# Optimization experiments

Hardware: AMD Instinct MI355X
Metric: run time of the kernel (lower is better)

## Reference

```python
import jax, jax.numpy as jnp
import numpy as np

B = 131072
SEQ = 64
HID = 20
LSTM_W_BITS = 8
LSTM_A_BITS = 6
LIN_W_BITS = 8
LIN_A_BITS = 6
IO_BITS = 8


def _ste(x, q):
    # straight-through estimator: forward value q, gradient of identity
    return x + jax.lax.stop_gradient(q - x)


def fq_signed_dyn(x, bits):
    # symmetric per-tensor fake quant, dynamic max-abs scale
    qmax = 2.0 ** (bits - 1) - 1.0
    s = jnp.maximum(jnp.max(jnp.abs(x)), 1e-8) / qmax
    q = jnp.clip(jnp.round(x / s), -qmax, qmax) * s
    return _ste(x, q)


def fq_unsigned_dyn(x, bits):
    # unsigned per-tensor fake quant (for post-ReLU activations)
    qmax = 2.0 ** bits - 1.0
    s = jnp.maximum(jnp.max(x), 1e-8) / qmax
    q = jnp.clip(jnp.round(x / s), 0.0, qmax) * s
    return _ste(x, q)


def fq_sigmoid(x, bits):
    # quantized sigmoid: output in [0,1], fixed scale 1/(2^b-1)
    qmax = 2.0 ** bits - 1.0
    y = jax.nn.sigmoid(x)
    return _ste(y, jnp.round(y * qmax) / qmax)


def fq_tanh(x, bits):
    # quantized tanh: output in [-1,1], fixed scale 1/(2^(b-1)-1)
    qmax = 2.0 ** (bits - 1) - 1.0
    y = jnp.tanh(x)
    return _ste(y, jnp.round(y * qmax) / qmax)


def setup_inputs() -> dict:
    key = jax.random.key(0)
    ks = jax.random.split(key, 10)

    def u(k, shape, fan_in):
        lim = 1.0 / np.sqrt(fan_in)
        return jax.random.uniform(k, shape, jnp.float32, -lim, lim)

    x = jax.random.normal(ks[0], (B, SEQ), jnp.float32)
    w_ih = u(ks[1], (4 * HID, 1), HID)      # LSTM input weights (input_size=1)
    w_hh = u(ks[2], (4 * HID, HID), HID)    # LSTM recurrent weights
    b = u(ks[3], (4 * HID,), HID)           # combined bias (bias_quant=None)
    W1 = u(ks[4], (64, HID), HID)
    b1 = u(ks[5], (64,), HID)
    W2 = u(ks[6], (32, 64), 64)
    b2 = u(ks[7], (32,), 64)
    W3 = u(ks[8], (4, 32), 32)
    b3 = u(ks[9], (4,), 32)
    return dict(x=x, w_ih=w_ih, w_hh=w_hh, b=b, W1=W1, b1=b1, W2=W2, b2=b2, W3=W3, b3=b3)


def reference(x, w_ih, w_hh, b, W1, b1, W2, b2, W3, b3):
    # io_quant (Int8ActPerTensorFloat) on LSTM input
    xq = fq_signed_dyn(x, IO_BITS)
    w_ih_q = fq_signed_dyn(w_ih, LSTM_W_BITS)
    w_hh_q = fq_signed_dyn(w_hh, LSTM_W_BITS)

    xs = xq.reshape(B, SEQ, 1).transpose(1, 0, 2)  # (SEQ, B, 1)

    def step(carry, x_t):
        h, c = carry
        gates = x_t @ w_ih_q.T + h @ w_hh_q.T + b   # (B, 4*HID)
        gates = fq_signed_dyn(gates, LSTM_A_BITS)   # gate_acc quant
        i_g, f_g, g_g, o_g = jnp.split(gates, 4, axis=-1)
        i = fq_sigmoid(i_g, LSTM_A_BITS)
        f = fq_sigmoid(f_g, LSTM_A_BITS)
        g = fq_tanh(g_g, LSTM_A_BITS)
        o = fq_sigmoid(o_g, LSTM_A_BITS)
        c_new = fq_signed_dyn(f * c + i * g, LSTM_A_BITS)  # cell_state quant
        h_new = o * fq_tanh(c_new, LSTM_A_BITS)
        return (h_new, c_new), None

    h0 = jnp.zeros((B, HID), jnp.float32)
    (h_last, _), _ = jax.lax.scan(step, (h0, h0), xs)

    # quantized MLP head: QuantReLU -> QuantLinear x3 -> ReLU
    out = fq_unsigned_dyn(jax.nn.relu(h_last), LIN_A_BITS)
    out = out @ fq_signed_dyn(W1, LIN_W_BITS).T + b1
    out = fq_unsigned_dyn(jax.nn.relu(out), LIN_A_BITS)
    out = out @ fq_signed_dyn(W2, LIN_W_BITS).T + b2
    out = fq_unsigned_dyn(jax.nn.relu(out), LIN_A_BITS)
    out = out @ fq_signed_dyn(W3, LIN_W_BITS).T + b3
    return jax.nn.relu(out)
```

## Files before the change

### kernel.cpp

```cpp
#include <hip/hip_runtime.h>
#include <math.h>


#define NBLK  256
#define NTHR  512
#define SEQL  64
#define HIDN  20
#define G4    80

typedef float f2 __attribute__((ext_vector_type(2)));
typedef unsigned long long u64;

__device__ __forceinline__ float tanh_xla(float x){
  const float kClamp = 7.90531110763549805f;
  float xc = fminf(fmaxf(x, -kClamp), kClamp);
  float x2 = xc*xc;
  float p = fmaf(x2, -2.76076847742355e-16f, 2.00018790482477e-13f);
  p = fmaf(x2, p, -8.60467152213735e-11f);
  p = fmaf(x2, p,  5.12229709037114e-08f);
  p = fmaf(x2, p,  1.48572235717979e-05f);
  p = fmaf(x2, p,  6.37261928875436e-04f);
  p = fmaf(x2, p,  4.89352455891786e-03f);
  p = p * xc;
  float q = fmaf(x2, 1.19825839466702e-06f, 1.18534705686654e-04f);
  q = fmaf(x2, q, 2.26843463243900e-03f);
  q = fmaf(x2, q, 4.89352518554385e-03f);
  float y = p / q;
  return (fabsf(x) < 4e-4f) ? x : y;
}

__device__ __forceinline__ float qround(float x, float s, float inv_s, float tol){
  float n = rintf(__fmul_rn(x, inv_s));
  float e = fmaf(-n, s, x);
  if (__builtin_expect(fabsf(fabsf(e) - 0.5f*s) <= tol*s, 0))
    n = rintf(x / s);
  return n;
}

__device__ __forceinline__ float phase_max(float lmax, int phase,
                                           u64* slots, int blk, int tid,
                                           volatile u64* s_red64,
                                           volatile u64* s_bc64)
{
  #pragma unroll
  for (int off=32; off; off>>=1) lmax = fmaxf(lmax, __shfl_xor(lmax, off, 64));
  const int wid = tid>>6, lane = tid&63;
  const unsigned int tag = (unsigned int)(phase+1);
  const u64 tw = ((u64)tag)<<32;
  if (lane==0) s_red64[wid] = tw | (u64)__float_as_uint(lmax);
  if (wid==0) {
    u64 pv = 0;
    if (lane<8) { do { pv = s_red64[lane]; } while ((unsigned int)(pv>>32)!=tag); }
    float bm = (lane<8) ? __uint_as_float((unsigned int)pv) : 0.f;
    bm = fmaxf(bm, __shfl_xor(bm,4,64));
    bm = fmaxf(bm, __shfl_xor(bm,2,64));
    bm = fmaxf(bm, __shfl_xor(bm,1,64));
    u64* sp = slots + (size_t)(phase&1)*NBLK;
    if (lane==0)
      __hip_atomic_store(sp+blk, tw | (u64)__float_as_uint(bm),
                         __ATOMIC_RELAXED, __HIP_MEMORY_SCOPE_AGENT);
    u64 v0,v1,v2,v3;
    for (;;) {
      v0 = __hip_atomic_load(sp+lane,     __ATOMIC_RELAXED, __HIP_MEMORY_SCOPE_AGENT);
      v1 = __hip_atomic_load(sp+lane+64,  __ATOMIC_RELAXED, __HIP_MEMORY_SCOPE_AGENT);
      v2 = __hip_atomic_load(sp+lane+128, __ATOMIC_RELAXED, __HIP_MEMORY_SCOPE_AGENT);
      v3 = __hip_atomic_load(sp+lane+192, __ATOMIC_RELAXED, __HIP_MEMORY_SCOPE_AGENT);
      bool ok = ((unsigned int)(v0>>32)==tag) && ((unsigned int)(v1>>32)==tag) &&
                ((unsigned int)(v2>>32)==tag) && ((unsigned int)(v3>>32)==tag);
      if (__all(ok)) break;
      __builtin_amdgcn_s_sleep(1);
    }
    unsigned int m0 = (unsigned int)v0, m1 = (unsigned int)v1;
    unsigned int m2 = (unsigned int)v2, m3 = (unsigned int)v3;
    unsigned int m = m0>m1?m0:m1; if (m2>m) m=m2; if (m3>m) m=m3;
    #pragma unroll
    for (int off=32; off; off>>=1) {
      unsigned int o = (unsigned int)__shfl_xor((int)m, off, 64);
      if (o>m) m=o;
    }
    if (lane==0) *s_bc64 = tw | (u64)m;
  }
  u64 bv;
  do { bv = *s_bc64; } while ((unsigned int)(bv>>32)!=tag);
  return __uint_as_float((unsigned int)bv);
}

__global__ void kinit(float* __restrict__ ws) {
  int i = threadIdx.x;
  for (; i < 1152; i += 256) ws[i] = 0.0f;
}

__global__ void kmaxabs_x(const float4* __restrict__ x4, int n4, int* __restrict__ xmax_bits) {
  float m = 0.f;
  int stride = gridDim.x*blockDim.x;
  for (int i = blockIdx.x*blockDim.x + threadIdx.x; i < n4; i += stride) {
    float4 v = x4[i];
    m = fmaxf(fmaxf(fabsf(v.x),fabsf(v.y)), fmaxf(fmaxf(fabsf(v.z),fabsf(v.w)), m));
  }
  #pragma unroll
  for (int off=32; off; off>>=1) m = fmaxf(m, __shfl_xor(m, off, 64));
  __shared__ float red[4];
  int wid = threadIdx.x>>6, lane = threadIdx.x&63;
  if (lane==0) red[wid]=m;
  __syncthreads();
  if (threadIdx.x==0) {
    float bm = fmaxf(fmaxf(red[0],red[1]), fmaxf(red[2],red[3]));
    atomicMax(xmax_bits, __float_as_int(bm));
  }
}

__global__ void kscales(const float* __restrict__ wih, const float* __restrict__ whh,
                        const float* __restrict__ W1, const float* __restrict__ W2,
                        const float* __restrict__ W3, float* __restrict__ ws)
{
  int wid = threadIdx.x>>6, lane = threadIdx.x&63;
  const float* p; int n;
  if      (wid==0){p=wih;n=80;}   else if (wid==1){p=whh;n=1600;}
  else if (wid==2){p=W1;n=1280;}  else if (wid==3){p=W2;n=2048;}
  else            {p=W3;n=128;}
  float m=0.f;
  for (int i=lane;i<n;i+=64) m=fmaxf(m,fabsf(p[i]));
  #pragma unroll
  for (int off=32; off; off>>=1) m=fmaxf(m,__shfl_xor(m,off,64));
  if (lane==0) ws[9+wid]=fmaxf(m,1e-8f)/127.0f;
  if (threadIdx.x==0) {
    float xm = __int_as_float(((const int*)ws)[0]);
    ws[8]=fmaxf(xm,1e-8f)/127.0f;
  }
}

__global__ void __launch_bounds__(NTHR, 2)
kmain(const float* __restrict__ x, const float* __restrict__ w_ih,
      const float* __restrict__ w_hh, const float* __restrict__ bias,
      const float* __restrict__ W1, const float* __restrict__ b1,
      const float* __restrict__ W2, const float* __restrict__ b2,
      const float* __restrict__ W3, const float* __restrict__ b3,
      float* __restrict__ out, float* __restrict__ ws)
{
  __shared__ float s_whh[HIDN*G4];
  __shared__ float s_wih[G4];
  __shared__ float s_b[G4];
  __shared__ float s_W1[HIDN*64];
  __shared__ float s_b1v[64];
  __shared__ float s_W2[64*32];
  __shared__ float s_b2v[32];
  __shared__ float s_W3[32*4];
  __shared__ float s_b3v[4];
  __shared__ float s_lutsig[63];
  __shared__ float s_luttg[63];
  __shared__ float s_luttc[63];
  __shared__ u64 s_red64[8];
  __shared__ u64 s_bc64;

  const int tid = threadIdx.x;
  const int blk = blockIdx.x;
  u64* slots = (u64*)(ws + 64);

  const float sx   = ws[8];
  const float swih = ws[9];
  const float swhh = ws[10];
  const float sw1  = ws[11];
  const float sw2  = ws[12];
  const float sw3  = ws[13];

  for (int i = tid; i < G4; i += NTHR) {
    s_wih[i] = fminf(fmaxf(rintf(w_ih[i]/swih), -127.f), 127.f)*swih;
    s_b[i]   = bias[i];
  }
  for (int i = tid; i < HIDN*G4; i += NTHR) {
    int j = i/HIDN, k = i - j*HIDN;
    s_whh[k*G4+j] = fminf(fmaxf(rintf(w_hh[i]/swhh), -127.f), 127.f)*swhh;
  }
  for (int i = tid; i < 64*HIDN; i += NTHR) {
    int j = i/HIDN, k = i - j*HIDN;
    s_W1[k*64+j] = fminf(fmaxf(rintf(W1[i]/sw1), -127.f), 127.f)*sw1;
  }
  for (int i = tid; i < 32*64; i += NTHR) {
    int j = i>>6, k = i&63;
    s_W2[k*32+j] = fminf(fmaxf(rintf(W2[i]/sw2), -127.f), 127.f)*sw2;
  }
  for (int i = tid; i < 4*32; i += NTHR) {
    int j = i>>5, k = i&31;
    s_W3[k*4+j] = fminf(fmaxf(rintf(W3[i]/sw3), -127.f), 127.f)*sw3;
  }
  if (tid < 64) s_b1v[tid] = b1[tid];
  if (tid < 32) s_b2v[tid] = b2[tid];
  if (tid < 4)  s_b3v[tid] = b3[tid];
  __syncthreads();

  const long bI = (long)blk*NTHR + tid;
  const float* xrow = x + bI*SEQL;
  const float inv_sx = __builtin_amdgcn_rcpf(sx);

  float h[HIDN], c[HIDN];
  #pragma unroll
  for (int k=0;k<HIDN;++k){ h[k]=0.f; c[k]=0.f; }

  float4 x4v;
  #pragma unroll 1
  for (int t=0; t<SEQL; ++t) {
    if ((t&3)==0) x4v = *(const float4*)(xrow + t);
    float xv = (t&3)==1 ? x4v.y : ((t&3)==2 ? x4v.z : ((t&3)==3 ? x4v.w : x4v.x));
    float xq = __fmul_rn(fminf(fmaxf(qround(xv, sx, inv_sx, 1e-4f), -127.f), 127.f), sx);

    f2 hw2[40];
    #pragma unroll
    for (int j=0;j<40;++j) { hw2[j].x = 0.f; hw2[j].y = 0.f; }
    #pragma unroll
    for (int k=0;k<HIDN;++k) {
      float hk = h[k];
      f2 hk2; hk2.x = hk; hk2.y = hk;
      const float4* w4 = (const float4*)&s_whh[k*G4];
      #pragma unroll
      for (int j4=0;j4<20;++j4) {
        float4 w = w4[j4];
        f2 wlo; wlo.x = w.x; wlo.y = w.y;
        f2 whi; whi.x = w.z; whi.y = w.w;
        hw2[2*j4]   = __builtin_elementwise_fma(hk2, wlo, hw2[2*j4]);
        hw2[2*j4+1] = __builtin_elementwise_fma(hk2, whi, hw2[2*j4+1]);
      }
    }
    float* hw = (float*)hw2;
    float lm = 0.f;
    #pragma unroll
    for (int j4=0;j4<20;++j4) {
      float4 wi = *(const float4*)&s_wih[j4*4];
      float4 bb = *(const float4*)&s_b[j4*4];
      float g0 = __fadd_rn(__fadd_rn(__fmul_rn(xq, wi.x), hw[j4*4  ]), bb.x);
      float g1 = __fadd_rn(__fadd_rn(__fmul_rn(xq, wi.y), hw[j4*4+1]), bb.y);
      float g2 = __fadd_rn(__fadd_rn(__fmul_rn(xq, wi.z), hw[j4*4+2]), bb.z);
      float g3 = __fadd_rn(__fadd_rn(__fmul_rn(xq, wi.w), hw[j4*4+3]), bb.w);
      hw[j4*4  ]=g0; hw[j4*4+1]=g1; hw[j4*4+2]=g2; hw[j4*4+3]=g3;
      lm = fmaxf(lm, fmaxf(fmaxf(fabsf(g0),fabsf(g1)), fmaxf(fabsf(g2),fabsf(g3))));
    }
    float gm = phase_max(lm, 2*t, slots, blk, tid, s_red64, &s_bc64);
    float s1 = fmaxf(gm, 1e-8f)/31.0f;
    float inv1 = __builtin_amdgcn_rcpf(s1);

    if (tid < 63) {
      float q  = __fmul_rn((float)(tid-31), s1);
      float ti = tanh_xla(0.5f*q);
      int ni = (int)rintf(fmaf(0.5f, ti, 0.5f)*63.0f);
      ni = min(max(ni,0),63);
      s_lutsig[tid] = (float)ni/63.0f;
    } else if (tid >= 64 && tid < 127) {
      int n = tid - 64 - 31;
      float q  = __fmul_rn((float)n, s1);
      float tg = tanh_xla(q);
      int ng = (int)rintf(tg*31.0f);
      ng = min(max(ng,-31),31);
      s_luttg[tid-64] = (float)ng/31.0f;
    }
    __syncthreads();

    float og[HIDN];
    float lm2 = 0.f;
    #pragma unroll
    for (int k=0;k<HIDN;++k) {
      int ii = min(max((int)qround(hw[k   ], s1, inv1, 2e-5f),-31),31)+31;
      int fi = min(max((int)qround(hw[20+k], s1, inv1, 2e-5f),-31),31)+31;
      int gi = min(max((int)qround(hw[40+k], s1, inv1, 2e-5f),-31),31)+31;
      int oi = min(max((int)qround(hw[60+k], s1, inv1, 2e-5f),-31),31)+31;
      float iv = s_lutsig[ii];
      float fv = s_lutsig[fi];
      float gv = s_luttg[gi];
      og[k]    = s_lutsig[oi];
      float pc = __fadd_rn(__fmul_rn(fv, c[k]), __fmul_rn(iv, gv));
      c[k] = pc;
      lm2 = fmaxf(lm2, fabsf(pc));
    }
    float gm2 = phase_max(lm2, 2*t+1, slots, blk, tid, s_red64, &s_bc64);
    float s2 = fmaxf(gm2, 1e-8f)/31.0f;
    float inv2 = __builtin_amdgcn_rcpf(s2);
    if (tid < 63) {
      float q  = __fmul_rn((float)(tid-31), s2);
      float tc = tanh_xla(q);
      int nc = (int)rintf(tc*31.0f);
      nc = min(max(nc,-31),31);
      s_luttc[tid] = (float)nc/31.0f;
    }
    __syncthreads();
    #pragma unroll
    for (int k=0;k<HIDN;++k) {
      int m = min(max((int)qround(c[k], s2, inv2, 2e-5f),-31),31);
      float cn = __fmul_rn((float)m, s2);
      c[k] = cn;
      h[k] = __fmul_rn(og[k], s_luttc[m+31]);
    }
  }

  float lm3 = 0.f;
  float a0[HIDN];
  #pragma unroll
  for (int k=0;k<HIDN;++k){ float r = fmaxf(h[k],0.f); a0[k]=r; lm3=fmaxf(lm3,r); }
  float gm3 = phase_max(lm3, 128, slots, blk, tid, s_red64, &s_bc64);
  float s3 = fmaxf(gm3,1e-8f)/63.0f;
  float inv3 = __builtin_amdgcn_rcpf(s3);
  #pragma unroll
  for (int k=0;k<HIDN;++k)
    a0[k] = __fmul_rn(fminf(fmaxf(qround(a0[k], s3, inv3, 4e-5f),0.f),63.f), s3);

  float o1[64];
  #pragma unroll
  for (int j=0;j<64;++j) o1[j] = 0.f;
  #pragma unroll
  for (int k=0;k<HIDN;++k) {
    float ak = a0[k];
    #pragma unroll
    for (int j=0;j<64;j+=4) {
      float4 w = *(const float4*)&s_W1[k*64+j];
      o1[j]   = fmaf(ak,w.x,o1[j]);
      o1[j+1] = fmaf(ak,w.y,o1[j+1]);
      o1[j+2] = fmaf(ak,w.z,o1[j+2]);
      o1[j+3] = fmaf(ak,w.w,o1[j+3]);
    }
  }
  float lm4 = 0.f;
  #pragma unroll
  for (int j=0;j<64;++j){ o1[j]=fmaxf(__fadd_rn(o1[j],s_b1v[j]),0.f); lm4=fmaxf(lm4,o1[j]); }
  float gm4 = phase_max(lm4, 129, slots, blk, tid, s_red64, &s_bc64);
  float s4 = fmaxf(gm4,1e-8f)/63.0f;
  float inv4 = __builtin_amdgcn_rcpf(s4);
  #pragma unroll
  for (int j=0;j<64;++j)
    o1[j] = __fmul_rn(fminf(fmaxf(qround(o1[j], s4, inv4, 4e-5f),0.f),63.f), s4);

  float o2[32];
  #pragma unroll
  for (int j=0;j<32;++j) o2[j] = 0.f;
  #pragma unroll
  for (int k=0;k<64;++k) {
    float ak = o1[k];
    #pragma unroll
    for (int j=0;j<32;j+=4) {
      float4 w = *(const float4*)&s_W2[k*32+j];
      o2[j]   = fmaf(ak,w.x,o2[j]);
      o2[j+1] = fmaf(ak,w.y,o2[j+1]);
      o2[j+2] = fmaf(ak,w.z,o2[j+2]);
      o2[j+3] = fmaf(ak,w.w,o2[j+3]);
    }
  }
  float lm5=0.f;
  #pragma unroll
  for (int j=0;j<32;++j){ o2[j]=fmaxf(__fadd_rn(o2[j],s_b2v[j]),0.f); lm5=fmaxf(lm5,o2[j]); }
  float gm5 = phase_max(lm5, 130, slots, blk, tid, s_red64, &s_bc64);
  float s5 = fmaxf(gm5,1e-8f)/63.0f;
  float inv5 = __builtin_amdgcn_rcpf(s5);
  #pragma unroll
  for (int j=0;j<32;++j)
    o2[j] = __fmul_rn(fminf(fmaxf(qround(o2[j], s5, inv5, 4e-5f),0.f),63.f), s5);

  float o3[4] = {0.f,0.f,0.f,0.f};
  #pragma unroll
  for (int k=0;k<32;++k) {
    float ak = o2[k];
    float4 w = *(const float4*)&s_W3[k*4];
    o3[0]=fmaf(ak,w.x,o3[0]); o3[1]=fmaf(ak,w.y,o3[1]);
    o3[2]=fmaf(ak,w.z,o3[2]); o3[3]=fmaf(ak,w.w,o3[3]);
  }
  float4 res;
  res.x = fmaxf(__fadd_rn(o3[0],s_b3v[0]),0.f);
  res.y = fmaxf(__fadd_rn(o3[1],s_b3v[1]),0.f);
  res.z = fmaxf(__fadd_rn(o3[2],s_b3v[2]),0.f);
  res.w = fmaxf(__fadd_rn(o3[3],s_b3v[3]),0.f);
  ((float4*)out)[bI] = res;
}

extern "C" void kernel_launch(void* const* d_in, const int* in_sizes, int n_in,
                              void* d_out, int out_size, void* d_ws, size_t ws_size,
                              hipStream_t stream) {
  const float* x    = (const float*)d_in[0];
  const float* w_ih = (const float*)d_in[1];
  const float* w_hh = (const float*)d_in[2];
  const float* b    = (const float*)d_in[3];
  const float* W1   = (const float*)d_in[4];
  const float* b1   = (const float*)d_in[5];
  const float* W2   = (const float*)d_in[6];
  const float* b2   = (const float*)d_in[7];
  const float* W3   = (const float*)d_in[8];
  const float* b3   = (const float*)d_in[9];
  float* out = (float*)d_out;
  float* ws  = (float*)d_ws;

  int n4 = in_sizes[0]/4;
  kinit<<<1,256,0,stream>>>(ws);
  kmaxabs_x<<<1024,256,0,stream>>>((const float4*)x, n4, (int*)ws);
  kscales<<<1,320,0,stream>>>(w_ih,w_hh,W1,W2,W3,ws);
  kmain<<<dim3(NBLK), dim3(NTHR), 0, stream>>>(x,w_ih,w_hh,b,W1,b1,W2,b2,W3,b3,out,ws);
}
```

Before: 1.326 ms.

## Process two batch rows per thread with half-size blocks in persistent LSTM kernel

Each thread now carries two independent LSTM sequences (NB=2) with 256-thread blocks instead of one sequence with 512 threads. Each shared-memory weight load of w_hh and the MLP weights is reused across two rows, which halves LDS traffic per row and gives more independent FMAs for latency hiding. The block-level reduction in the grid-wide max barrier now involves 4 waves instead of 8, and the slot publish uses an atomic exchange instead of a store. The cost is roughly double register pressure (two h/c states and two 80-wide gate accumulators), hence launch bounds relaxed to 1 block per CU, which risks spills or lower occupancy.

```diff
diff --git a/kernel.cpp b/kernel.cpp
--- a/kernel.cpp
+++ b/kernel.cpp
@@ -3,7 +3,8 @@
 
 
 #define NBLK  256
-#define NTHR  512
+#define NTHR  256
+#define NB    2
 #define SEQL  64
 #define HIDN  20
 #define G4    80
@@ -50,15 +51,14 @@
   if (lane==0) s_red64[wid] = tw | (u64)__float_as_uint(lmax);
   if (wid==0) {
     u64 pv = 0;
-    if (lane<8) { do { pv = s_red64[lane]; } while ((unsigned int)(pv>>32)!=tag); }
-    float bm = (lane<8) ? __uint_as_float((unsigned int)pv) : 0.f;
-    bm = fmaxf(bm, __shfl_xor(bm,4,64));
+    if (lane<4) { do { pv = s_red64[lane]; } while ((unsigned int)(pv>>32)!=tag); }
+    float bm = (lane<4) ? __uint_as_float((unsigned int)pv) : 0.f;
     bm = fmaxf(bm, __shfl_xor(bm,2,64));
     bm = fmaxf(bm, __shfl_xor(bm,1,64));
     u64* sp = slots + (size_t)(phase&1)*NBLK;
     if (lane==0)
-      __hip_atomic_store(sp+blk, tw | (u64)__float_as_uint(bm),
-                         __ATOMIC_RELAXED, __HIP_MEMORY_SCOPE_AGENT);
+      (void)__hip_atomic_exchange(sp+blk, tw | (u64)__float_as_uint(bm),
+                                  __ATOMIC_RELAXED, __HIP_MEMORY_SCOPE_AGENT);
     u64 v0,v1,v2,v3;
     for (;;) {
       v0 = __hip_atomic_load(sp+lane,     __ATOMIC_RELAXED, __HIP_MEMORY_SCOPE_AGENT);
@@ -129,7 +129,7 @@
   }
 }
 
-__global__ void __launch_bounds__(NTHR, 2)
+__global__ void __launch_bounds__(NTHR, 1)
 kmain(const float* __restrict__ x, const float* __restrict__ w_ih,
       const float* __restrict__ w_hh, const float* __restrict__ bias,
       const float* __restrict__ W1, const float* __restrict__ b1,
@@ -149,7 +149,7 @@
   __shared__ float s_lutsig[63];
   __shared__ float s_luttg[63];
   __shared__ float s_luttc[63];
-  __shared__ u64 s_red64[8];
+  __shared__ u64 s_red64[4];
   __shared__ u64 s_bc64;
 
   const int tid = threadIdx.x;
@@ -188,50 +188,66 @@
   if (tid < 4)  s_b3v[tid] = b3[tid];
   __syncthreads();
 
-  const long bI = (long)blk*NTHR + tid;
-  const float* xrow = x + bI*SEQL;
+  const long e0 = (long)blk*(NTHR*NB) + tid;
+  const long e1 = e0 + NTHR;
+  const float* xr0 = x + e0*SEQL;
+  const float* xr1 = x + e1*SEQL;
   const float inv_sx = __builtin_amdgcn_rcpf(sx);
 
-  float h[HIDN], c[HIDN];
-  #pragma unroll
-  for (int k=0;k<HIDN;++k){ h[k]=0.f; c[k]=0.f; }
-
-  float4 x4v;
+  float h[NB][HIDN], c[NB][HIDN];
+  #pragma unroll
+  for (int e=0;e<NB;++e)
+    #pragma unroll
+    for (int k=0;k<HIDN;++k){ h[e][k]=0.f; c[e][k]=0.f; }
+
+  float4 xv0, xv1;
   #pragma unroll 1
   for (int t=0; t<SEQL; ++t) {
-    if ((t&3)==0) x4v = *(const float4*)(xrow + t);
-    float xv = (t&3)==1 ? x4v.y : ((t&3)==2 ? x4v.z : ((t&3)==3 ? x4v.w : x4v.x));
-    float xq = __fmul_rn(fminf(fmaxf(qround(xv, sx, inv_sx, 1e-4f), -127.f), 127.f), sx);
-
-    f2 hw2[40];
-    #pragma unroll
-    for (int j=0;j<40;++j) { hw2[j].x = 0.f; hw2[j].y = 0.f; }
+    if ((t&3)==0) { xv0 = *(const float4*)(xr0 + t); xv1 = *(const float4*)(xr1 + t); }
+    float xa = (t&3)==1 ? xv0.y : ((t&3)==2 ? xv0.z : ((t&3)==3 ? xv0.w : xv0.x));
+    float xb = (t&3)==1 ? xv1.y : ((t&3)==2 ? xv1.z : ((t&3)==3 ? xv1.w : xv1.x));
+    float xq[NB];
+    xq[0] = __fmul_rn(fminf(fmaxf(qround(xa, sx, inv_sx, 1e-4f), -127.f), 127.f), sx);
+    xq[1] = __fmul_rn(fminf(fmaxf(qround(xb, sx, inv_sx, 1e-4f), -127.f), 127.f), sx);
+
+    f2 hw2[NB][40];
+    #pragma unroll
+    for (int e=0;e<NB;++e)
+      #pragma unroll
+      for (int j=0;j<40;++j) { hw2[e][j].x = 0.f; hw2[e][j].y = 0.f; }
     #pragma unroll
     for (int k=0;k<HIDN;++k) {
-      float hk = h[k];
-      f2 hk2; hk2.x = hk; hk2.y = hk;
+      f2 hk2[NB];
+      #pragma unroll
+      for (int e=0;e<NB;++e) { hk2[e].x = h[e][k]; hk2[e].y = h[e][k]; }
       const float4* w4 = (const float4*)&s_whh[k*G4];
       #pragma unroll
       for (int j4=0;j4<20;++j4) {
         float4 w = w4[j4];
         f2 wlo; wlo.x = w.x; wlo.y = w.y;
         f2 whi; whi.x = w.z; whi.y = w.w;
-        hw2[2*j4]   = __builtin_elementwise_fma(hk2, wlo, hw2[2*j4]);
-        hw2[2*j4+1] = __builtin_elementwise_fma(hk2, whi, hw2[2*j4+1]);
-      }
-    }
-    float* hw = (float*)hw2;
+        #pragma unroll
+        for (int e=0;e<NB;++e) {
+          hw2[e][2*j4]   = __builtin_elementwise_fma(hk2[e], wlo, hw2[e][2*j4]);
+          hw2[e][2*j4+1] = __builtin_elementwise_fma(hk2[e], whi, hw2[e][2*j4+1]);
+        }
+      }
+    }
     float lm = 0.f;
     #pragma unroll
     for (int j4=0;j4<20;++j4) {
       float4 wi = *(const float4*)&s_wih[j4*4];
       float4 bb = *(const float4*)&s_b[j4*4];
-      float g0 = __fadd_rn(__fadd_rn(__fmul_rn(xq, wi.x), hw[j4*4  ]), bb.x);
-      float g1 = __fadd_rn(__fadd_rn(__fmul_rn(xq, wi.y), hw[j4*4+1]), bb.y);
-      float g2 = __fadd_rn(__fadd_rn(__fmul_rn(xq, wi.z), hw[j4*4+2]), bb.z);
-      float g3 = __fadd_rn(__fadd_rn(__fmul_rn(xq, wi.w), hw[j4*4+3]), bb.w);
-      hw[j4*4  ]=g0; hw[j4*4+1]=g1; hw[j4*4+2]=g2; hw[j4*4+3]=g3;
-      lm = fmaxf(lm, fmaxf(fmaxf(fabsf(g0),fabsf(g1)), fmaxf(fabsf(g2),fabsf(g3))));
+      #pragma unroll
+      for (int e=0;e<NB;++e) {
+        float* hw = (float*)hw2[e];
+        float g0 = __fadd_rn(__fadd_rn(__fmul_rn(xq[e], wi.x), hw[j4*4  ]), bb.x);
+        float g1 = __fadd_rn(__fadd_rn(__fmul_rn(xq[e], wi.y), hw[j4*4+1]), bb.y);
+        float g2 = __fadd_rn(__fadd_rn(__fmul_rn(xq[e], wi.z), hw[j4*4+2]), bb.z);
+        float g3 = __fadd_rn(__fadd_rn(__fmul_rn(xq[e], wi.w), hw[j4*4+3]), bb.w);
+        hw[j4*4  ]=g0; hw[j4*4+1]=g1; hw[j4*4+2]=g2; hw[j4*4+3]=g3;
+        lm = fmaxf(lm, fmaxf(fmaxf(fabsf(g0),fabsf(g1)), fmaxf(fabsf(g2),fabsf(g3))));
+      }
     }
     float gm = phase_max(lm, 2*t, slots, blk, tid, s_red64, &s_bc64);
     float s1 = fmaxf(gm, 1e-8f)/31.0f;
@@ -253,21 +269,25 @@
     }
     __syncthreads();
 
-    float og[HIDN];
+    float og[NB][HIDN];
     float lm2 = 0.f;
     #pragma unroll
-    for (int k=0;k<HIDN;++k) {
-      int ii = min(max((int)qround(hw[k   ], s1, inv1, 2e-5f),-31),31)+31;
-      int fi = min(max((int)qround(hw[20+k], s1, inv1, 2e-5f),-31),31)+31;
-      int gi = min(max((int)qround(hw[40+k], s1, inv1, 2e-5f),-31),31)+31;
-      int oi = min(max((int)qround(hw[60+k], s1, inv1, 2e-5f),-31),31)+31;
-      float iv = s_lutsig[ii];
-      float fv = s_lutsig[fi];
-      float gv = s_luttg[gi];
-      og[k]    = s_lutsig[oi];
-      float pc = __fadd_rn(__fmul_rn(fv, c[k]), __fmul_rn(iv, gv));
-      c[k] = pc;
-      lm2 = fmaxf(lm2, fabsf(pc));
+    for (int e=0;e<NB;++e) {
+      float* hw = (float*)hw2[e];
+      #pragma unroll
+      for (int k=0;k<HIDN;++k) {
+        int ii = min(max((int)qround(hw[k   ], s1, inv1, 2e-5f),-31),31)+31;
+        int fi = min(max((int)qround(hw[20+k], s1, inv1, 2e-5f),-31),31)+31;
+        int gi = min(max((int)qround(hw[40+k], s1, inv1, 2e-5f),-31),31)+31;
+        int oi = min(max((int)qround(hw[60+k], s1, inv1, 2e-5f),-31),31)+31;
+        float iv = s_lutsig[ii];
+        float fv = s_lutsig[fi];
+        float gv = s_luttg[gi];
+        og[e][k] = s_lutsig[oi];
+        float pc = __fadd_rn(__fmul_rn(fv, c[e][k]), __fmul_rn(iv, gv));
+        c[e][k] = pc;
+        lm2 = fmaxf(lm2, fabsf(pc));
+      }
     }
     float gm2 = phase_max(lm2, 2*t+1, slots, blk, tid, s_red64, &s_bc64);
     float s2 = fmaxf(gm2, 1e-8f)/31.0f;
@@ -281,89 +301,123 @@
     }
     __syncthreads();
     #pragma unroll
-    for (int k=0;k<HIDN;++k) {
-      int m = min(max((int)qround(c[k], s2, inv2, 2e-5f),-31),31);
-      float cn = __fmul_rn((float)m, s2);
-      c[k] = cn;
-      h[k] = __fmul_rn(og[k], s_luttc[m+31]);
-    }
+    for (int e=0;e<NB;++e)
+      #pragma unroll
+      for (int k=0;k<HIDN;++k) {
+        int m = min(max((int)qround(c[e][k], s2, inv2, 2e-5f),-31),31);
+        float cn = __fmul_rn((float)m, s2);
+        c[e][k] = cn;
+        h[e][k] = __fmul_rn(og[e][k], s_luttc[m+31]);
+      }
   }
 
   float lm3 = 0.f;
-  float a0[HIDN];
-  #pragma unroll
-  for (int k=0;k<HIDN;++k){ float r = fmaxf(h[k],0.f); a0[k]=r; lm3=fmaxf(lm3,r); }
+  float a0[NB][HIDN];
+  #pragma unroll
+  for (int e=0;e<NB;++e)
+    #pragma unroll
+    for (int k=0;k<HIDN;++k){ float r = fmaxf(h[e][k],0.f); a0[e][k]=r; lm3=fmaxf(lm3,r); }
   float gm3 = phase_max(lm3, 128, slots, blk, tid, s_red64, &s_bc64);
   float s3 = fmaxf(gm3,1e-8f)/63.0f;
   float inv3 = __builtin_amdgcn_rcpf(s3);
   #pragma unroll
-  for (int k=0;k<HIDN;++k)
-    a0[k] = __fmul_rn(fminf(fmaxf(qround(a0[k], s3, inv3, 4e-5f),0.f),63.f), s3);
-
-  float o1[64];
-  #pragma unroll
-  for (int j=0;j<64;++j) o1[j] = 0.f;
+  for (int e=0;e<NB;++e)
+    #pragma unroll
+    for (int k=0;k<HIDN;++k)
+      a0[e][k] = __fmul_rn(fminf(fmaxf(qround(a0[e][k], s3, inv3, 4e-5f),0.f),63.f), s3);
+
+  float o1[NB][64];
+  #pragma unroll
+  for (int e=0;e<NB;++e)
+    #pragma unroll
+    for (int j=0;j<64;++j) o1[e][j] = 0.f;
   #pragma unroll
   for (int k=0;k<HIDN;++k) {
-    float ak = a0[k];
     #pragma unroll
     for (int j=0;j<64;j+=4) {
       float4 w = *(const float4*)&s_W1[k*64+j];
-      o1[j]   = fmaf(ak,w.x,o1[j]);
-      o1[j+1] = fmaf(ak,w.y,o1[j+1]);
-      o1[j+2] = fmaf(ak,w.z,o1[j+2]);
-      o1[j+3] = fmaf(ak,w.w,o1[j+3]);
+      #pragma unroll
+      for (int e=0;e<NB;++e) {
+        float ak = a0[e][k];
+        o1[e][j]   = fmaf(ak,w.x,o1[e][j]);
+        o1[e][j+1] = fmaf(ak,w.y,o1[e][j+1]);
+        o1[e][j+2] = fmaf(ak,w.z,o1[e][j+2]);
+        o1[e][j+3] = fmaf(ak,w.w,o1[e][j+3]);
+      }
     }
   }
   float lm4 = 0.f;
   #pragma unroll
-  for (int j=0;j<64;++j){ o1[j]=fmaxf(__fadd_rn(o1[j],s_b1v[j]),0.f); lm4=fmaxf(lm4,o1[j]); }
+  for (int e=0;e<NB;++e)
+    #pragma unroll
+    for (int j=0;j<64;++j){ o1[e][j]=fmaxf(__fadd_rn(o1[e][j],s_b1v[j]),0.f); lm4=fmaxf(lm4,o1[e][j]); }
   float gm4 = phase_max(lm4, 129, slots, blk, tid, s_red64, &s_bc64);
   float s4 = fmaxf(gm4,1e-8f)/63.0f;
   float inv4 = __builtin_amdgcn_rcpf(s4);
   #pragma unroll
-  for (int j=0;j<64;++j)
-    o1[j] = __fmul_rn(fminf(fmaxf(qround(o1[j], s4, inv4, 4e-5f),0.f),63.f), s4);
-
-  float o2[32];
-  #pragma unroll
-  for (int j=0;j<32;++j) o2[j] = 0.f;
+  for (int e=0;e<NB;++e)
+    #pragma unroll
+    for (int j=0;j<64;++j)
+      o1[e][j] = __fmul_rn(fminf(fmaxf(qround(o1[e][j], s4, inv4, 4e-5f),0.f),63.f), s4);
+
+  float o2[NB][32];
+  #pragma unroll
+  for (int e=0;e<NB;++e)
+    #pragma unroll
+    for (int j=0;j<32;++j) o2[e][j] = 0.f;
   #pragma unroll
   for (int k=0;k<64;++k) {
-    float ak = o1[k];
     #pragma unroll
     for (int j=0;j<32;j+=4) {
       float4 w = *(const float4*)&s_W2[k*32+j];
-      o2[j]   = fmaf(ak,w.x,o2[j]);
-      o2[j+1] = fmaf(ak,w.y,o2[j+1]);
-      o2[j+2] = fmaf(ak,w.z,o2[j+2]);
-      o2[j+3] = fmaf(ak,w.w,o2[j+3]);
+      #pragma unroll
+      for (int e=0;e<NB;++e) {
+        float ak = o1[e][k];
+        o2[e][j]   = fmaf(ak,w.x,o2[e][j]);
+        o2[e][j+1] = fmaf(ak,w.y,o2[e][j+1]);
+        o2[e][j+2] = fmaf(ak,w.z,o2[e][j+2]);
+        o2[e][j+3] = fmaf(ak,w.w,o2[e][j+3]);
+      }
     }
   }
   float lm5=0.f;
   #pragma unroll
-  for (int j=0;j<32;++j){ o2[j]=fmaxf(__fadd_rn(o2[j],s_b2v[j]),0.f); lm5=fmaxf(lm5,o2[j]); }
+  for (int e=0;e<NB;++e)
+    #pragma unroll
+    for (int j=0;j<32;++j){ o2[e][j]=fmaxf(__fadd_rn(o2[e][j],s_b2v[j]),0.f); lm5=fmaxf(lm5,o2[e][j]); }
   float gm5 = phase_max(lm5, 130, slots, blk, tid, s_red64, &s_bc64);
   float s5 = fmaxf(gm5,1e-8f)/63.0f;
   float inv5 = __builtin_amdgcn_rcpf(s5);
   #pragma unroll
-  for (int j=0;j<32;++j)
-    o2[j] = __fmul_rn(fminf(fmaxf(qround(o2[j], s5, inv5, 4e-5f),0.f),63.f), s5);
-
-  float o3[4] = {0.f,0.f,0.f,0.f};
+  for (int e=0;e<NB;++e)
+    #pragma unroll
+    for (int j=0;j<32;++j)
+      o2[e][j] = __fmul_rn(fminf(fmaxf(qround(o2[e][j], s5, inv5, 4e-5f),0.f),63.f), s5);
+
+  float o3[NB][4];
+  #pragma unroll
+  for (int e=0;e<NB;++e) { o3[e][0]=0.f; o3[e][1]=0.f; o3[e][2]=0.f; o3[e][3]=0.f; }
   #pragma unroll
   for (int k=0;k<32;++k) {
-    float ak = o2[k];
     float4 w = *(const float4*)&s_W3[k*4];
-    o3[0]=fmaf(ak,w.x,o3[0]); o3[1]=fmaf(ak,w.y,o3[1]);
-    o3[2]=fmaf(ak,w.z,o3[2]); o3[3]=fmaf(ak,w.w,o3[3]);
-  }
-  float4 res;
-  res.x = fmaxf(__fadd_rn(o3[0],s_b3v[0]),0.f);
-  res.y = fmaxf(__fadd_rn(o3[1],s_b3v[1]),0.f);
-  res.z = fmaxf(__fadd_rn(o3[2],s_b3v[2]),0.f);
-  res.w = fmaxf(__fadd_rn(o3[3],s_b3v[3]),0.f);
-  ((float4*)out)[bI] = res;
+    #pragma unroll
+    for (int e=0;e<NB;++e) {
+      float ak = o2[e][k];
+      o3[e][0]=fmaf(ak,w.x,o3[e][0]); o3[e][1]=fmaf(ak,w.y,o3[e][1]);
+      o3[e][2]=fmaf(ak,w.z,o3[e][2]); o3[e][3]=fmaf(ak,w.w,o3[e][3]);
+    }
+  }
+  float4 r0, r1;
+  r0.x = fmaxf(__fadd_rn(o3[0][0],s_b3v[0]),0.f);
+  r0.y = fmaxf(__fadd_rn(o3[0][1],s_b3v[1]),0.f);
+  r0.z = fmaxf(__fadd_rn(o3[0][2],s_b3v[2]),0.f);
+  r0.w = fmaxf(__fadd_rn(o3[0][3],s_b3v[3]),0.f);
+  r1.x = fmaxf(__fadd_rn(o3[1][0],s_b3v[0]),0.f);
+  r1.y = fmaxf(__fadd_rn(o3[1][1],s_b3v[1]),0.f);
+  r1.z = fmaxf(__fadd_rn(o3[1][2],s_b3v[2]),0.f);
+  r1.w = fmaxf(__fadd_rn(o3[1][3],s_b3v[3]),0.f);
+  ((float4*)out)[e0] = r0;
+  ((float4*)out)[e1] = r1;
 }
 
 extern "C" void kernel_launch(void* const* d_in, const int* in_sizes, int n_in,
```

Result: slower. 2.046 ms (+54.4%).

## Replace per-block slot grid barrier with atomic max plus arrival counter

Applied to the files above, without the earlier changes.

The cross-block max reduction used in every phase changes. Previously each block wrote a tagged value into a 256-entry slot array, and a whole wavefront polled all slots. Now each block does one atomic fetch-max into a per-phase value and one atomic increment of a shared arrival counter, and only lane 0 spins until the counter reaches phase_count*NBLK. This cuts polling traffic and the final shuffle reduction, at the cost of 256 blocks contending on the same atomic addresses each phase. The workspace init is shrunk to match the smaller layout.

```diff
diff --git a/kernel.cpp b/kernel.cpp
--- a/kernel.cpp
+++ b/kernel.cpp
@@ -38,7 +38,8 @@
 }
 
 __device__ __forceinline__ float phase_max(float lmax, int phase,
-                                           u64* slots, int blk, int tid,
+                                           unsigned int* cnt, unsigned int* vals,
+                                           int tid,
                                            volatile u64* s_red64,
                                            volatile u64* s_bc64)
 {
@@ -55,30 +56,21 @@
     bm = fmaxf(bm, __shfl_xor(bm,4,64));
     bm = fmaxf(bm, __shfl_xor(bm,2,64));
     bm = fmaxf(bm, __shfl_xor(bm,1,64));
-    u64* sp = slots + (size_t)(phase&1)*NBLK;
-    if (lane==0)
-      __hip_atomic_store(sp+blk, tw | (u64)__float_as_uint(bm),
-                         __ATOMIC_RELAXED, __HIP_MEMORY_SCOPE_AGENT);
-    u64 v0,v1,v2,v3;
-    for (;;) {
-      v0 = __hip_atomic_load(sp+lane,     __ATOMIC_RELAXED, __HIP_MEMORY_SCOPE_AGENT);
-      v1 = __hip_atomic_load(sp+lane+64,  __ATOMIC_RELAXED, __HIP_MEMORY_SCOPE_AGENT);
-      v2 = __hip_atomic_load(sp+lane+128, __ATOMIC_RELAXED, __HIP_MEMORY_SCOPE_AGENT);
-      v3 = __hip_atomic_load(sp+lane+192, __ATOMIC_RELAXED, __HIP_MEMORY_SCOPE_AGENT);
-      bool ok = ((unsigned int)(v0>>32)==tag) && ((unsigned int)(v1>>32)==tag) &&
-                ((unsigned int)(v2>>32)==tag) && ((unsigned int)(v3>>32)==tag);
-      if (__all(ok)) break;
-      __builtin_amdgcn_s_sleep(1);
-    }
-    unsigned int m0 = (unsigned int)v0, m1 = (unsigned int)v1;
-    unsigned int m2 = (unsigned int)v2, m3 = (unsigned int)v3;
-    unsigned int m = m0>m1?m0:m1; if (m2>m) m=m2; if (m3>m) m=m3;
-    #pragma unroll
-    for (int off=32; off; off>>=1) {
-      unsigned int o = (unsigned int)__shfl_xor((int)m, off, 64);
-      if (o>m) m=o;
-    }
-    if (lane==0) *s_bc64 = tw | (u64)m;
+    if (lane==0) {
+      unsigned int old = __hip_atomic_fetch_max(vals+phase, __float_as_uint(bm),
+                              __ATOMIC_RELAXED, __HIP_MEMORY_SCOPE_AGENT);
+      __asm__ volatile("" :: "v"(old));
+      (void)__hip_atomic_fetch_add(cnt, 1u, __ATOMIC_RELAXED, __HIP_MEMORY_SCOPE_AGENT);
+      const unsigned int target = tag*(unsigned int)NBLK;
+      unsigned int c;
+      for (;;) {
+        c = __hip_atomic_load(cnt, __ATOMIC_RELAXED, __HIP_MEMORY_SCOPE_AGENT);
+        if (c >= target) break;
+        __builtin_amdgcn_s_sleep(1);
+      }
+      unsigned int m = __hip_atomic_load(vals+phase, __ATOMIC_RELAXED, __HIP_MEMORY_SCOPE_AGENT);
+      *s_bc64 = tw | (u64)m;
+    }
   }
   u64 bv;
   do { bv = *s_bc64; } while ((unsigned int)(bv>>32)!=tag);
@@ -87,7 +79,7 @@
 
 __global__ void kinit(float* __restrict__ ws) {
   int i = threadIdx.x;
-  for (; i < 1152; i += 256) ws[i] = 0.0f;
+  for (; i < 256; i += 256) ws[i] = 0.0f;
 }
 
 __global__ void kmaxabs_x(const float4* __restrict__ x4, int n4, int* __restrict__ xmax_bits) {
@@ -154,7 +146,8 @@
 
   const int tid = threadIdx.x;
   const int blk = blockIdx.x;
-  u64* slots = (u64*)(ws + 64);
+  unsigned int* cnt  = (unsigned int*)(ws + 16);
+  unsigned int* vals = (unsigned int*)(ws + 32);
 
   const float sx   = ws[8];
   const float swih = ws[9];
@@ -233,7 +226,7 @@
       hw[j4*4  ]=g0; hw[j4*4+1]=g1; hw[j4*4+2]=g2; hw[j4*4+3]=g3;
       lm = fmaxf(lm, fmaxf(fmaxf(fabsf(g0),fabsf(g1)), fmaxf(fabsf(g2),fabsf(g3))));
     }
-    float gm = phase_max(lm, 2*t, slots, blk, tid, s_red64, &s_bc64);
+    float gm = phase_max(lm, 2*t, cnt, vals, tid, s_red64, &s_bc64);
     float s1 = fmaxf(gm, 1e-8f)/31.0f;
     float inv1 = __builtin_amdgcn_rcpf(s1);
 
@@ -269,7 +262,7 @@
       c[k] = pc;
       lm2 = fmaxf(lm2, fabsf(pc));
     }
-    float gm2 = phase_max(lm2, 2*t+1, slots, blk, tid, s_red64, &s_bc64);
+    float gm2 = phase_max(lm2, 2*t+1, cnt, vals, tid, s_red64, &s_bc64);
     float s2 = fmaxf(gm2, 1e-8f)/31.0f;
     float inv2 = __builtin_amdgcn_rcpf(s2);
     if (tid < 63) {
@@ -293,7 +286,7 @@
   float a0[HIDN];
   #pragma unroll
   for (int k=0;k<HIDN;++k){ float r = fmaxf(h[k],0.f); a0[k]=r; lm3=fmaxf(lm3,r); }
-  float gm3 = phase_max(lm3, 128, slots, blk, tid, s_red64, &s_bc64);
+  float gm3 = phase_max(lm3, 128, cnt, vals, tid, s_red64, &s_bc64);
   float s3 = fmaxf(gm3,1e-8f)/63.0f;
   float inv3 = __builtin_amdgcn_rcpf(s3);
   #pragma unroll
@@ -318,7 +311,7 @@
   float lm4 = 0.f;
   #pragma unroll
   for (int j=0;j<64;++j){ o1[j]=fmaxf(__fadd_rn(o1[j],s_b1v[j]),0.f); lm4=fmaxf(lm4,o1[j]); }
-  float gm4 = phase_max(lm4, 129, slots, blk, tid, s_red64, &s_bc64);
+  float gm4 = phase_max(lm4, 129, cnt, vals, tid, s_red64, &s_bc64);
   float s4 = fmaxf(gm4,1e-8f)/63.0f;
   float inv4 = __builtin_amdgcn_rcpf(s4);
   #pragma unroll
@@ -343,7 +336,7 @@
   float lm5=0.f;
   #pragma unroll
   for (int j=0;j<32;++j){ o2[j]=fmaxf(__fadd_rn(o2[j],s_b2v[j]),0.f); lm5=fmaxf(lm5,o2[j]); }
-  float gm5 = phase_max(lm5, 130, slots, blk, tid, s_red64, &s_bc64);
+  float gm5 = phase_max(lm5, 130, cnt, vals, tid, s_red64, &s_bc64);
   float s5 = fmaxf(gm5,1e-8f)/63.0f;
   float inv5 = __builtin_amdgcn_rcpf(s5);
   #pragma unroll
```

Result: slower. 2.128 ms (+60.5%).
